# Performance work log

Hardware: AMD Instinct MI355X
Metric: run time of the kernel (lower is better)

## Reference

```python
import jax, jax.numpy as jnp
import numpy as np

B, S, D, F, E = 4, 2048, 1024, 4096, 8

def setup_inputs() -> dict:
    key = jax.random.key(0)
    ks = jax.random.split(key, 5)
    x = jax.random.normal(ks[0], (B, S, D), dtype=jnp.float32)
    router_w = jax.random.normal(ks[1], (D, E), dtype=jnp.float32) * (D ** -0.5)
    router_b = jnp.zeros((E,), dtype=jnp.float32)
    w1 = jax.random.normal(ks[2], (E, F, D), dtype=jnp.float32) * (D ** -0.5)
    b1 = jnp.zeros((E, F), dtype=jnp.float32)
    w2 = jax.random.normal(ks[3], (E, D, F), dtype=jnp.float32) * (F ** -0.5)
    b2 = jnp.zeros((E, D), dtype=jnp.float32)
    return {"x": x, "router_w": router_w, "router_b": router_b,
            "w1": w1, "b1": b1, "w2": w2, "b2": b2}

def reference(x, router_w, router_b, w1, b1, w2, b2):
    # Router: mean over sequence, linear, softmax -> [B, E]
    routing_probs = jax.nn.softmax(jnp.mean(x, axis=1) @ router_w + router_b, axis=-1)
    # SMEAR merge weights: mean over batch -> [E] (dropout is identity, p=0)
    ew = jnp.mean(routing_probs, axis=0)
    # Batched weighted sum of stacked expert parameters (fuses the python loop)
    mw1 = jnp.einsum('e,efd->fd', ew, w1)   # [F, D]
    mb1 = ew @ b1                            # [F]
    mw2 = jnp.einsum('e,edf->df', ew, w2)   # [D, F]
    mb2 = ew @ b2                            # [D]
    # functional_call on merged expert (MLP with GELU)
    h = jax.nn.gelu(jnp.einsum('bsd,fd->bsf', x, mw1) + mb1)
    out = jnp.einsum('bsf,df->bsd', h, mw2) + mb2
    return out
```

## Files before the change

kernel.cpp:

```cpp
#include <hip/hip_runtime.h>
#include <hip/hip_bf16.h>
#include <stdint.h>

#define B_ 4
#define S_ 2048
#define D_ 1024
#define F_ 4096
#define E_ 8

typedef __attribute__((ext_vector_type(4))) float f32x4;
typedef __attribute__((ext_vector_type(8))) short bf16x8;

__device__ __forceinline__ unsigned short f2bf(float f) {
    union { float f; unsigned int u; } v; v.f = f;
    unsigned int r = v.u + 0x7fffu + ((v.u >> 16) & 1u);
    return (unsigned short)(r >> 16);
}

__device__ __forceinline__ float gelu_tanh(float x) {
    const float c0 = 0.7978845608028654f;
    const float c1 = 0.044715f;
    float x3 = x * x * x;
    return 0.5f * x * (1.0f + tanhf(c0 * (x + c1 * x3)));
}

__global__ void prep_x_kernel(const float* __restrict__ x,
                              unsigned short* __restrict__ xb,
                              float* __restrict__ xsum) {
    const int b = blockIdx.y;
    const int t = threadIdx.x;
    const int d0 = t * 4;
    const float* xbase = x + (size_t)b * S_ * D_;
    unsigned short* obase = xb + (size_t)b * S_ * D_;
    float s0 = 0.f, s1 = 0.f, s2 = 0.f, s3 = 0.f;
    for (int s = blockIdx.x; s < S_; s += gridDim.x) {
        f32x4 v = *(const f32x4*)(xbase + (size_t)s * D_ + d0);
        ushort4 o;
        o.x = f2bf(v.x); o.y = f2bf(v.y); o.z = f2bf(v.z); o.w = f2bf(v.w);
        *(ushort4*)(obase + (size_t)s * D_ + d0) = o;
        s0 += v.x; s1 += v.y; s2 += v.z; s3 += v.w;
    }
    atomicAdd(&xsum[b * D_ + d0 + 0], s0);
    atomicAdd(&xsum[b * D_ + d0 + 1], s1);
    atomicAdd(&xsum[b * D_ + d0 + 2], s2);
    atomicAdd(&xsum[b * D_ + d0 + 3], s3);
}

__global__ void router_kernel(const float* __restrict__ xsum,
                              const float* __restrict__ rw,
                              const float* __restrict__ rb,
                              float* __restrict__ ew) {
    __shared__ float logits[B_][E_];
    __shared__ float probs[B_][E_];
    const int t = threadIdx.x;
    const int b = t >> 6;
    const int e = (t >> 3) & 7;
    const int part = t & 7;
    float s = 0.f;
    const int dbeg = part * (D_ / 8);
    for (int d = dbeg; d < dbeg + D_ / 8; ++d)
        s += xsum[b * D_ + d] * rw[d * E_ + e];
    s += __shfl_down(s, 4);
    s += __shfl_down(s, 2);
    s += __shfl_down(s, 1);
    if (part == 0) logits[b][e] = s * (1.0f / S_) + rb[e];
    __syncthreads();
    if (t < B_) {
        float mx = -1e30f;
        for (int j = 0; j < E_; ++j) mx = fmaxf(mx, logits[t][j]);
        float sum = 0.f;
        float ex[E_];
        for (int j = 0; j < E_; ++j) { ex[j] = expf(logits[t][j] - mx); sum += ex[j]; }
        for (int j = 0; j < E_; ++j) probs[t][j] = ex[j] / sum;
    }
    __syncthreads();
    if (t < E_) {
        float m = 0.f;
        for (int j = 0; j < B_; ++j) m += probs[j][t];
        ew[t] = m * (1.0f / B_);
    }
}

__global__ void merge_w_kernel(const float* __restrict__ w, const float* __restrict__ ew,
                               unsigned short* __restrict__ dst, int n) {
    float e[E_];
#pragma unroll
    for (int i = 0; i < E_; ++i) e[i] = ew[i];
    const size_t total = (size_t)n >> 2;
    for (size_t q = (size_t)blockIdx.x * blockDim.x + threadIdx.x; q < total;
         q += (size_t)gridDim.x * blockDim.x) {
        f32x4 acc = {0.f, 0.f, 0.f, 0.f};
#pragma unroll
        for (int i = 0; i < E_; ++i) {
            f32x4 v = *(const f32x4*)(w + (size_t)i * n + q * 4);
            acc += v * e[i];
        }
        ushort4 o;
        o.x = f2bf(acc.x); o.y = f2bf(acc.y); o.z = f2bf(acc.z); o.w = f2bf(acc.w);
        *(ushort4*)(dst + q * 4) = o;
    }
}

__global__ void merge_biases(const float* __restrict__ b1, const float* __restrict__ b2,
                             const float* __restrict__ ew,
                             float* __restrict__ mb1, float* __restrict__ mb2) {
    const int i = blockIdx.x * blockDim.x + threadIdx.x;
    float e[E_];
#pragma unroll
    for (int j = 0; j < E_; ++j) e[j] = ew[j];
    if (i < F_) {
        float a = 0.f;
#pragma unroll
        for (int j = 0; j < E_; ++j) a += e[j] * b1[(size_t)j * F_ + i];
        mb1[i] = a;
    } else if (i - F_ < D_) {
        const int i2 = i - F_;
        float a = 0.f;
#pragma unroll
        for (int j = 0; j < E_; ++j) a += e[j] * b2[(size_t)j * D_ + i2];
        mb2[i2] = a;
    }
}

__global__ void init_out_kernel(float* __restrict__ out, const float* __restrict__ mb2) {
    const size_t total_q = (size_t)B_ * S_ * D_ / 4;
    for (size_t q = (size_t)blockIdx.x * blockDim.x + threadIdx.x; q < total_q;
         q += (size_t)gridDim.x * blockDim.x) {
        ((f32x4*)out)[q] = ((const f32x4*)mb2)[q & (D_ / 4 - 1)];
    }
}

#define LGKM0() do { asm volatile("s_waitcnt lgkmcnt(0)" ::: "memory"); \
                     __builtin_amdgcn_sched_barrier(0); } while (0)
#define VMCNT(n) asm volatile("s_waitcnt vmcnt(" #n ")" ::: "memory")
#define BARRIER() __builtin_amdgcn_s_barrier()

template <int EPI>
__global__ __launch_bounds__(512, 2) void gemm256(const unsigned short* __restrict__ A,
                                                  const unsigned short* __restrict__ Bm,
                                                  const float* __restrict__ bias,
                                                  void* __restrict__ Cout0,
                                                  int M, int N, int K, int Klen) {
    __shared__ __align__(128) char lds[131072];
    const int tid = threadIdx.x;
    const int wave = tid >> 6, lane = tid & 63;
    const int wr = wave >> 2, wc = wave & 3;
    const int row0 = blockIdx.y * 256, col0 = blockIdx.x * 256;
    const int kt0 = blockIdx.z * Klen;
    const int NI = Klen / 128;

    const int c0 = tid, c1 = tid + 512;
    const int r0c = ((c0 >> 7) << 4) | ((c0 >> 2) & 15);
    const int k0c = (((c0 >> 6) & 1) << 5) | ((((c0 & 3) << 3) ^ (((c0 >> 5) & 1) << 4)));
    const int r1c = ((c1 >> 7) << 4) | ((c1 >> 2) & 15);
    const int k1c = (((c1 >> 6) & 1) << 5) | ((((c1 & 3) << 3) ^ (((c1 >> 5) & 1) << 4)));
    const size_t soff0 = (size_t)r0c * K + k0c;
    const size_t soff1 = (size_t)r1c * K + k1c;

    const unsigned short* pA0 = A + (size_t)row0 * K + kt0;
    const unsigned short* pA1 = pA0 + (size_t)128 * K;
    const unsigned short* pB0 = Bm + (size_t)col0 * K + kt0;
    const unsigned short* pB1 = pB0 + (size_t)128 * K;

    int lane_off = ((lane & 15) << 6) + ((lane >> 4) << 4);
    lane_off ^= (lane & 8) << 2;
    const int wrOff = wr * 16384;
    const int wcOff = 32768 + (wc >> 1) * 16384 + (wc & 1) * 8192;

    f32x4 acc[8][4];
#pragma unroll
    for (int m = 0; m < 8; ++m)
#pragma unroll
        for (int n = 0; n < 4; ++n) acc[m][n] = (f32x4){0.f, 0.f, 0.f, 0.f};
    bf16x8 aF[4][2], bF[4][2];

#define STAGE(ptr, ktb, ldsoff) do { \
    __builtin_amdgcn_global_load_lds((const __attribute__((address_space(1))) void*)((ptr) + (ktb) + soff0), \
        (__attribute__((address_space(3))) void*)(lds + (ldsoff) + wave * 1024), 16, 0, 0); \
    __builtin_amdgcn_global_load_lds((const __attribute__((address_space(1))) void*)((ptr) + (ktb) + soff1), \
        (__attribute__((address_space(3))) void*)(lds + (ldsoff) + wave * 1024 + 8192), 16, 0, 0); \
  } while (0)

#define RDA4(MB, BUFB) do { _Pragma("unroll") for (int m = 0; m < 4; ++m) { \
    aF[m][0] = *(const bf16x8*)(lds + (BUFB) + wrOff + ((MB) + m) * 2048 + lane_off); \
    aF[m][1] = *(const bf16x8*)(lds + (BUFB) + wrOff + ((MB) + m) * 2048 + 1024 + lane_off); } } while (0)

#define RDB2(NB, BUFB) do { _Pragma("unroll") for (int n = 0; n < 2; ++n) { \
    bF[(NB) + n][0] = *(const bf16x8*)(lds + (BUFB) + wcOff + ((NB) + n) * 2048 + lane_off); \
    bF[(NB) + n][1] = *(const bf16x8*)(lds + (BUFB) + wcOff + ((NB) + n) * 2048 + 1024 + lane_off); } } while (0)

#define MFMAQ(MB, NB) do { \
    __builtin_amdgcn_s_setprio(1); \
    _Pragma("unroll") for (int m = 0; m < 4; ++m) \
    _Pragma("unroll") for (int n = 0; n < 2; ++n) \
    _Pragma("unroll") for (int ks = 0; ks < 2; ++ks) \
      acc[(MB) + m][(NB) + n] = __builtin_amdgcn_mfma_f32_16x16x32_bf16( \
          aF[m][ks], bF[(NB) + n][ks], acc[(MB) + m][(NB) + n], 0, 0, 0); \
    __builtin_amdgcn_s_setprio(0); \
  } while (0)

    STAGE(pA0, 0, 0);
    STAGE(pA1, 0, 16384);
    STAGE(pB0, 0, 32768);
    STAGE(pB1, 0, 49152);
    STAGE(pB0, 64, 65536 + 32768);
    STAGE(pB1, 64, 65536 + 49152);

    for (int i = 0; i < NI; ++i) {
        const int t = 2 * i;
        const int ktN1 = (t + 1) * 64, ktN2 = (t + 2) * 64, ktN3 = (t + 3) * 64;
        const bool last = (i == NI - 1);

        VMCNT(4);
        BARRIER();
        RDA4(0, 0); RDB2(0, 0);
        STAGE(pA0, ktN1, 65536);
        LGKM0();
        MFMAQ(0, 0);
        RDB2(2, 0);
        STAGE(pA1, ktN1, 65536 + 16384);
        LGKM0();
        MFMAQ(0, 2);
        BARRIER();
        RDA4(4, 0);
        if (!last) STAGE(pB0, ktN2, 32768);
        LGKM0();
        MFMAQ(4, 2);
        if (!last) STAGE(pB1, ktN2, 49152);
        MFMAQ(4, 0);
        if (last) { VMCNT(0); } else { VMCNT(4); }
        BARRIER();
        RDA4(0, 65536); RDB2(0, 65536);
        if (!last) STAGE(pA0, ktN2, 0);
        LGKM0();
        MFMAQ(0, 0);
        RDB2(2, 65536);
        if (!last) STAGE(pA1, ktN2, 16384);
        LGKM0();
        MFMAQ(0, 2);
        BARRIER();
        RDA4(4, 65536);
        if (!last) STAGE(pB0, ktN3, 65536 + 32768);
        LGKM0();
        MFMAQ(4, 2);
        if (!last) STAGE(pB1, ktN3, 65536 + 49152);
        MFMAQ(4, 0);
    }

    const int fr = lane & 15, fq = lane >> 4;
    if (EPI == 0) {
        unsigned short* dst = (unsigned short*)Cout0;
#pragma unroll
        for (int n = 0; n < 4; ++n) {
            const int c = col0 + wc * 64 + n * 16 + fr;
            const float bv = bias[c];
#pragma unroll
            for (int m = 0; m < 8; ++m) {
                const int rb = row0 + wr * 128 + m * 16 + fq * 4;
#pragma unroll
                for (int v = 0; v < 4; ++v) {
                    float val = acc[m][n][v] + bv;
                    dst[(size_t)(rb + v) * N + c] = f2bf(gelu_tanh(val));
                }
            }
        }
    } else {
        float* dst = (float*)Cout0;
#pragma unroll
        for (int n = 0; n < 4; ++n) {
            const int c = col0 + wc * 64 + n * 16 + fr;
#pragma unroll
            for (int m = 0; m < 8; ++m) {
                const int rb = row0 + wr * 128 + m * 16 + fq * 4;
#pragma unroll
                for (int v = 0; v < 4; ++v)
                    atomicAdd(&dst[(size_t)(rb + v) * N + c], acc[m][n][v]);
            }
        }
    }
#undef STAGE
#undef RDA4
#undef RDB2
#undef MFMAQ
}

extern "C" void kernel_launch(void* const* d_in, const int* in_sizes, int n_in,
                              void* d_out, int out_size, void* d_ws, size_t ws_size,
                              hipStream_t stream) {
    const float* x  = (const float*)d_in[0];
    const float* rw = (const float*)d_in[1];
    const float* rb = (const float*)d_in[2];
    const float* w1 = (const float*)d_in[3];
    const float* b1 = (const float*)d_in[4];
    const float* w2 = (const float*)d_in[5];
    const float* b2 = (const float*)d_in[6];
    float* out = (float*)d_out;

    char* p = (char*)d_ws;
    auto take = [&](size_t bytes) { char* r = p; p += (bytes + 255) & ~(size_t)255; return r; };
    float* xsum          = (float*)take((size_t)B_ * D_ * sizeof(float));
    float* ew            = (float*)take(E_ * sizeof(float));
    float* mb1           = (float*)take(F_ * sizeof(float));
    float* mb2           = (float*)take(D_ * sizeof(float));
    unsigned short* xb   = (unsigned short*)take((size_t)B_ * S_ * D_ * 2);
    unsigned short* mw1b = (unsigned short*)take((size_t)F_ * D_ * 2);
    unsigned short* mw2b = (unsigned short*)take((size_t)D_ * F_ * 2);
    unsigned short* h    = (unsigned short*)take((size_t)B_ * S_ * F_ * 2);

    hipMemsetAsync(xsum, 0, (size_t)B_ * D_ * sizeof(float), stream);
    prep_x_kernel<<<dim3(128, B_), 256, 0, stream>>>(x, xb, xsum);
    router_kernel<<<1, 256, 0, stream>>>(xsum, rw, rb, ew);
    merge_w_kernel<<<2048, 256, 0, stream>>>(w1, ew, mw1b, F_ * D_);
    merge_w_kernel<<<2048, 256, 0, stream>>>(w2, ew, mw2b, D_ * F_);
    merge_biases<<<(F_ + D_) / 256, 256, 0, stream>>>(b1, b2, ew, mb1, mb2);
    init_out_kernel<<<2048, 256, 0, stream>>>(out, mb2);
    gemm256<0><<<dim3(F_ / 256, (B_ * S_) / 256, 1), 512, 0, stream>>>(
        xb, mw1b, mb1, h, B_ * S_, F_, D_, D_);
    gemm256<3><<<dim3(D_ / 256, (B_ * S_) / 256, 2), 512, 0, stream>>>(
        h, mw2b, nullptr, out, B_ * S_, D_, F_, F_ / 2);
}
```

Baseline: 564.2 us.

## Replace split-K atomic GEMM2 with 128-row tile GEMM, fuse merge kernels, swizzle blocks

Swaps the second GEMM's split-K atomicAdd scheme for a new 128x256 tile kernel that writes output plus bias directly, which removes the init_out pass and the atomic traffic. Both GEMMs gain an XCD-style workgroup swizzle aimed at better L2 reuse. The two weight merges and the bias merge are fused into one launch. GELU's tanhf is replaced by an exp-based formula. The smaller tile lowers per-block reuse, and the fast exp changes numerics slightly.

```diff
diff --git a/kernel.cpp b/kernel.cpp
--- a/kernel.cpp
+++ b/kernel.cpp
@@ -20,8 +20,9 @@
 __device__ __forceinline__ float gelu_tanh(float x) {
     const float c0 = 0.7978845608028654f;
     const float c1 = 0.044715f;
-    float x3 = x * x * x;
-    return 0.5f * x * (1.0f + tanhf(c0 * (x + c1 * x3)));
+    float u = c0 * (x + c1 * x * x * x);
+    float t = 1.0f - 2.0f / (__expf(2.0f * u) + 1.0f);
+    return 0.5f * x * (1.0f + t);
 }
 
 __global__ void prep_x_kernel(const float* __restrict__ x,
@@ -81,14 +82,23 @@
     }
 }
 
-__global__ void merge_w_kernel(const float* __restrict__ w, const float* __restrict__ ew,
-                               unsigned short* __restrict__ dst, int n) {
+__global__ void merge_all_kernel(const float* __restrict__ w1, const float* __restrict__ w2,
+                                 const float* __restrict__ b1, const float* __restrict__ b2,
+                                 const float* __restrict__ ew,
+                                 unsigned short* __restrict__ mw1b, unsigned short* __restrict__ mw2b,
+                                 float* __restrict__ mb1, float* __restrict__ mb2) {
     float e[E_];
 #pragma unroll
     for (int i = 0; i < E_; ++i) e[i] = ew[i];
-    const size_t total = (size_t)n >> 2;
-    for (size_t q = (size_t)blockIdx.x * blockDim.x + threadIdx.x; q < total;
-         q += (size_t)gridDim.x * blockDim.x) {
+    const size_t n = (size_t)F_ * D_;
+    const size_t nq = n >> 2;
+    const int half = gridDim.x >> 1;
+    const bool first = (int)blockIdx.x < half;
+    const float* w = first ? w1 : w2;
+    unsigned short* dst = first ? mw1b : mw2b;
+    const int bid = first ? blockIdx.x : blockIdx.x - half;
+    for (size_t q = (size_t)bid * blockDim.x + threadIdx.x; q < nq;
+         q += (size_t)half * blockDim.x) {
         f32x4 acc = {0.f, 0.f, 0.f, 0.f};
 #pragma unroll
         for (int i = 0; i < E_; ++i) {
@@ -99,34 +109,21 @@
         o.x = f2bf(acc.x); o.y = f2bf(acc.y); o.z = f2bf(acc.z); o.w = f2bf(acc.w);
         *(ushort4*)(dst + q * 4) = o;
     }
-}
-
-__global__ void merge_biases(const float* __restrict__ b1, const float* __restrict__ b2,
-                             const float* __restrict__ ew,
-                             float* __restrict__ mb1, float* __restrict__ mb2) {
-    const int i = blockIdx.x * blockDim.x + threadIdx.x;
-    float e[E_];
-#pragma unroll
-    for (int j = 0; j < E_; ++j) e[j] = ew[j];
-    if (i < F_) {
-        float a = 0.f;
-#pragma unroll
-        for (int j = 0; j < E_; ++j) a += e[j] * b1[(size_t)j * F_ + i];
-        mb1[i] = a;
-    } else if (i - F_ < D_) {
-        const int i2 = i - F_;
-        float a = 0.f;
-#pragma unroll
-        for (int j = 0; j < E_; ++j) a += e[j] * b2[(size_t)j * D_ + i2];
-        mb2[i2] = a;
-    }
-}
-
-__global__ void init_out_kernel(float* __restrict__ out, const float* __restrict__ mb2) {
-    const size_t total_q = (size_t)B_ * S_ * D_ / 4;
-    for (size_t q = (size_t)blockIdx.x * blockDim.x + threadIdx.x; q < total_q;
-         q += (size_t)gridDim.x * blockDim.x) {
-        ((f32x4*)out)[q] = ((const f32x4*)mb2)[q & (D_ / 4 - 1)];
+    if (blockIdx.x == gridDim.x - 1) {
+        for (int i = threadIdx.x; i < F_ + D_; i += blockDim.x) {
+            if (i < F_) {
+                float a = 0.f;
+#pragma unroll
+                for (int j = 0; j < E_; ++j) a += e[j] * b1[(size_t)j * F_ + i];
+                mb1[i] = a;
+            } else {
+                const int i2 = i - F_;
+                float a = 0.f;
+#pragma unroll
+                for (int j = 0; j < E_; ++j) a += e[j] * b2[(size_t)j * D_ + i2];
+                mb2[i2] = a;
+            }
+        }
     }
 }
 
@@ -135,19 +132,21 @@
 #define VMCNT(n) asm volatile("s_waitcnt vmcnt(" #n ")" ::: "memory")
 #define BARRIER() __builtin_amdgcn_s_barrier()
 
-template <int EPI>
 __global__ __launch_bounds__(512, 2) void gemm256(const unsigned short* __restrict__ A,
                                                   const unsigned short* __restrict__ Bm,
                                                   const float* __restrict__ bias,
-                                                  void* __restrict__ Cout0,
-                                                  int M, int N, int K, int Klen) {
+                                                  unsigned short* __restrict__ Cout,
+                                                  int M, int N, int K) {
     __shared__ __align__(128) char lds[131072];
     const int tid = threadIdx.x;
     const int wave = tid >> 6, lane = tid & 63;
     const int wr = wave >> 2, wc = wave & 3;
-    const int row0 = blockIdx.y * 256, col0 = blockIdx.x * 256;
-    const int kt0 = blockIdx.z * Klen;
-    const int NI = Klen / 128;
+    const int nbx = N / 256;
+    const int wg = blockIdx.y * nbx + blockIdx.x;
+    const int nwg = (M / 256) * nbx;
+    const int swz = (wg & 7) * (nwg >> 3) + (wg >> 3);
+    const int row0 = (swz / nbx) * 256, col0 = (swz % nbx) * 256;
+    const int NI = K / 128;
 
     const int c0 = tid, c1 = tid + 512;
     const int r0c = ((c0 >> 7) << 4) | ((c0 >> 2) & 15);
@@ -157,9 +156,9 @@
     const size_t soff0 = (size_t)r0c * K + k0c;
     const size_t soff1 = (size_t)r1c * K + k1c;
 
-    const unsigned short* pA0 = A + (size_t)row0 * K + kt0;
+    const unsigned short* pA0 = A + (size_t)row0 * K;
     const unsigned short* pA1 = pA0 + (size_t)128 * K;
-    const unsigned short* pB0 = Bm + (size_t)col0 * K + kt0;
+    const unsigned short* pB0 = Bm + (size_t)col0 * K;
     const unsigned short* pB1 = pB0 + (size_t)128 * K;
 
     int lane_off = ((lane & 15) << 6) + ((lane >> 4) << 4);
@@ -174,22 +173,22 @@
         for (int n = 0; n < 4; ++n) acc[m][n] = (f32x4){0.f, 0.f, 0.f, 0.f};
     bf16x8 aF[4][2], bF[4][2];
 
-#define STAGE(ptr, ktb, ldsoff) do { \
+#define STAGE6(ptr, ktb, ldsoff) do { \
     __builtin_amdgcn_global_load_lds((const __attribute__((address_space(1))) void*)((ptr) + (ktb) + soff0), \
         (__attribute__((address_space(3))) void*)(lds + (ldsoff) + wave * 1024), 16, 0, 0); \
     __builtin_amdgcn_global_load_lds((const __attribute__((address_space(1))) void*)((ptr) + (ktb) + soff1), \
         (__attribute__((address_space(3))) void*)(lds + (ldsoff) + wave * 1024 + 8192), 16, 0, 0); \
   } while (0)
 
-#define RDA4(MB, BUFB) do { _Pragma("unroll") for (int m = 0; m < 4; ++m) { \
+#define RDA46(MB, BUFB) do { _Pragma("unroll") for (int m = 0; m < 4; ++m) { \
     aF[m][0] = *(const bf16x8*)(lds + (BUFB) + wrOff + ((MB) + m) * 2048 + lane_off); \
     aF[m][1] = *(const bf16x8*)(lds + (BUFB) + wrOff + ((MB) + m) * 2048 + 1024 + lane_off); } } while (0)
 
-#define RDB2(NB, BUFB) do { _Pragma("unroll") for (int n = 0; n < 2; ++n) { \
+#define RDB26(NB, BUFB) do { _Pragma("unroll") for (int n = 0; n < 2; ++n) { \
     bF[(NB) + n][0] = *(const bf16x8*)(lds + (BUFB) + wcOff + ((NB) + n) * 2048 + lane_off); \
     bF[(NB) + n][1] = *(const bf16x8*)(lds + (BUFB) + wcOff + ((NB) + n) * 2048 + 1024 + lane_off); } } while (0)
 
-#define MFMAQ(MB, NB) do { \
+#define MFMAQ6(MB, NB) do { \
     __builtin_amdgcn_s_setprio(1); \
     _Pragma("unroll") for (int m = 0; m < 4; ++m) \
     _Pragma("unroll") for (int n = 0; n < 2; ++n) \
@@ -199,12 +198,12 @@
     __builtin_amdgcn_s_setprio(0); \
   } while (0)
 
-    STAGE(pA0, 0, 0);
-    STAGE(pA1, 0, 16384);
-    STAGE(pB0, 0, 32768);
-    STAGE(pB1, 0, 49152);
-    STAGE(pB0, 64, 65536 + 32768);
-    STAGE(pB1, 64, 65536 + 49152);
+    STAGE6(pA0, 0, 0);
+    STAGE6(pA1, 0, 16384);
+    STAGE6(pB0, 0, 32768);
+    STAGE6(pB1, 0, 49152);
+    STAGE6(pB0, 64, 65536 + 32768);
+    STAGE6(pB1, 64, 65536 + 49152);
 
     for (int i = 0; i < NI; ++i) {
         const int t = 2 * i;
@@ -213,75 +212,194 @@
 
         VMCNT(4);
         BARRIER();
-        RDA4(0, 0); RDB2(0, 0);
-        STAGE(pA0, ktN1, 65536);
-        LGKM0();
-        MFMAQ(0, 0);
-        RDB2(2, 0);
-        STAGE(pA1, ktN1, 65536 + 16384);
-        LGKM0();
-        MFMAQ(0, 2);
-        BARRIER();
-        RDA4(4, 0);
-        if (!last) STAGE(pB0, ktN2, 32768);
-        LGKM0();
-        MFMAQ(4, 2);
-        if (!last) STAGE(pB1, ktN2, 49152);
-        MFMAQ(4, 0);
+        RDA46(0, 0); RDB26(0, 0);
+        STAGE6(pA0, ktN1, 65536);
+        LGKM0();
+        MFMAQ6(0, 0);
+        RDB26(2, 0);
+        STAGE6(pA1, ktN1, 65536 + 16384);
+        LGKM0();
+        MFMAQ6(0, 2);
+        BARRIER();
+        RDA46(4, 0);
+        if (!last) STAGE6(pB0, ktN2, 32768);
+        LGKM0();
+        MFMAQ6(4, 2);
+        if (!last) STAGE6(pB1, ktN2, 49152);
+        MFMAQ6(4, 0);
         if (last) { VMCNT(0); } else { VMCNT(4); }
         BARRIER();
-        RDA4(0, 65536); RDB2(0, 65536);
-        if (!last) STAGE(pA0, ktN2, 0);
-        LGKM0();
-        MFMAQ(0, 0);
-        RDB2(2, 65536);
-        if (!last) STAGE(pA1, ktN2, 16384);
-        LGKM0();
-        MFMAQ(0, 2);
-        BARRIER();
-        RDA4(4, 65536);
-        if (!last) STAGE(pB0, ktN3, 65536 + 32768);
-        LGKM0();
-        MFMAQ(4, 2);
-        if (!last) STAGE(pB1, ktN3, 65536 + 49152);
-        MFMAQ(4, 0);
+        RDA46(0, 65536); RDB26(0, 65536);
+        if (!last) STAGE6(pA0, ktN2, 0);
+        LGKM0();
+        MFMAQ6(0, 0);
+        RDB26(2, 65536);
+        if (!last) STAGE6(pA1, ktN2, 16384);
+        LGKM0();
+        MFMAQ6(0, 2);
+        BARRIER();
+        RDA46(4, 65536);
+        if (!last) STAGE6(pB0, ktN3, 65536 + 32768);
+        LGKM0();
+        MFMAQ6(4, 2);
+        if (!last) STAGE6(pB1, ktN3, 65536 + 49152);
+        MFMAQ6(4, 0);
     }
 
     const int fr = lane & 15, fq = lane >> 4;
-    if (EPI == 0) {
-        unsigned short* dst = (unsigned short*)Cout0;
-#pragma unroll
-        for (int n = 0; n < 4; ++n) {
-            const int c = col0 + wc * 64 + n * 16 + fr;
-            const float bv = bias[c];
-#pragma unroll
-            for (int m = 0; m < 8; ++m) {
-                const int rb = row0 + wr * 128 + m * 16 + fq * 4;
-#pragma unroll
-                for (int v = 0; v < 4; ++v) {
-                    float val = acc[m][n][v] + bv;
-                    dst[(size_t)(rb + v) * N + c] = f2bf(gelu_tanh(val));
-                }
+#pragma unroll
+    for (int n = 0; n < 4; ++n) {
+        const int c = col0 + wc * 64 + n * 16 + fr;
+        const float bv = bias[c];
+#pragma unroll
+        for (int m = 0; m < 8; ++m) {
+            const int rb = row0 + wr * 128 + m * 16 + fq * 4;
+#pragma unroll
+            for (int v = 0; v < 4; ++v) {
+                float val = acc[m][n][v] + bv;
+                Cout[(size_t)(rb + v) * N + c] = f2bf(gelu_tanh(val));
             }
         }
-    } else {
-        float* dst = (float*)Cout0;
-#pragma unroll
-        for (int n = 0; n < 4; ++n) {
-            const int c = col0 + wc * 64 + n * 16 + fr;
-#pragma unroll
-            for (int m = 0; m < 8; ++m) {
-                const int rb = row0 + wr * 128 + m * 16 + fq * 4;
-#pragma unroll
-                for (int v = 0; v < 4; ++v)
-                    atomicAdd(&dst[(size_t)(rb + v) * N + c], acc[m][n][v]);
-            }
+    }
+#undef STAGE6
+#undef RDA46
+#undef RDB26
+#undef MFMAQ6
+}
+
+__global__ __launch_bounds__(512, 2) void gemm128(const unsigned short* __restrict__ A,
+                                                  const unsigned short* __restrict__ Bm,
+                                                  const float* __restrict__ bias,
+                                                  float* __restrict__ Cout,
+                                                  int M, int N, int K) {
+    __shared__ __align__(128) char lds[98304];
+    const int tid = threadIdx.x;
+    const int wave = tid >> 6, lane = tid & 63;
+    const int wr = wave >> 2, wc = wave & 3;
+    const int nbx = N / 256;
+    const int wg = blockIdx.y * nbx + blockIdx.x;
+    const int nwg = (M / 128) * nbx;
+    const int swz = (wg & 7) * (nwg >> 3) + (wg >> 3);
+    const int row0 = (swz / nbx) * 128, col0 = (swz % nbx) * 256;
+    const int NI = K / 128;
+
+    const int c0 = tid, c1 = tid + 512;
+    const int r0c = ((c0 >> 7) << 4) | ((c0 >> 2) & 15);
+    const int k0c = (((c0 >> 6) & 1) << 5) | ((((c0 & 3) << 3) ^ (((c0 >> 5) & 1) << 4)));
+    const int r1c = ((c1 >> 7) << 4) | ((c1 >> 2) & 15);
+    const int k1c = (((c1 >> 6) & 1) << 5) | ((((c1 & 3) << 3) ^ (((c1 >> 5) & 1) << 4)));
+    const size_t soff0 = (size_t)r0c * K + k0c;
+    const size_t soff1 = (size_t)r1c * K + k1c;
+
+    const unsigned short* pA  = A + (size_t)row0 * K;
+    const unsigned short* pB0 = Bm + (size_t)col0 * K;
+    const unsigned short* pB1 = pB0 + (size_t)128 * K;
+
+    int lane_off = ((lane & 15) << 6) + ((lane >> 4) << 4);
+    lane_off ^= (lane & 8) << 2;
+    const int wcOff = (wc >> 1) * 16384 + (wc & 1) * 8192;
+
+    f32x4 acc[4][4];
+#pragma unroll
+    for (int m = 0; m < 4; ++m)
+#pragma unroll
+        for (int n = 0; n < 4; ++n) acc[m][n] = (f32x4){0.f, 0.f, 0.f, 0.f};
+    bf16x8 aF[2][2], bF[4][2];
+
+#define A0OFF 0
+#define B0OFF 16384
+#define A1OFF 49152
+#define B1OFF 65536
+
+#define STAGE1(ptr, ktb, ldsoff) do { \
+    __builtin_amdgcn_global_load_lds((const __attribute__((address_space(1))) void*)((ptr) + (ktb) + soff0), \
+        (__attribute__((address_space(3))) void*)(lds + (ldsoff) + wave * 1024), 16, 0, 0); \
+    __builtin_amdgcn_global_load_lds((const __attribute__((address_space(1))) void*)((ptr) + (ktb) + soff1), \
+        (__attribute__((address_space(3))) void*)(lds + (ldsoff) + wave * 1024 + 8192), 16, 0, 0); \
+  } while (0)
+
+#define RDA2(MB, ABASE) do { _Pragma("unroll") for (int j = 0; j < 2; ++j) { \
+    aF[j][0] = *(const bf16x8*)(lds + (ABASE) + (wr * 4 + (MB) + j) * 2048 + lane_off); \
+    aF[j][1] = *(const bf16x8*)(lds + (ABASE) + (wr * 4 + (MB) + j) * 2048 + 1024 + lane_off); } } while (0)
+
+#define RDB2X(NB, BBASE) do { _Pragma("unroll") for (int n = 0; n < 2; ++n) { \
+    bF[(NB) + n][0] = *(const bf16x8*)(lds + (BBASE) + wcOff + ((NB) + n) * 2048 + lane_off); \
+    bF[(NB) + n][1] = *(const bf16x8*)(lds + (BBASE) + wcOff + ((NB) + n) * 2048 + 1024 + lane_off); } } while (0)
+
+#define MFMAQ2(MB, NB) do { \
+    __builtin_amdgcn_s_setprio(1); \
+    _Pragma("unroll") for (int j = 0; j < 2; ++j) \
+    _Pragma("unroll") for (int n = 0; n < 2; ++n) \
+    _Pragma("unroll") for (int ks = 0; ks < 2; ++ks) \
+      acc[(MB) + j][(NB) + n] = __builtin_amdgcn_mfma_f32_16x16x32_bf16( \
+          aF[j][ks], bF[(NB) + n][ks], acc[(MB) + j][(NB) + n], 0, 0, 0); \
+    __builtin_amdgcn_s_setprio(0); \
+  } while (0)
+
+    STAGE1(pA, 0, A0OFF);
+    STAGE1(pB0, 0, B0OFF);
+    STAGE1(pB1, 0, B0OFF + 16384);
+    STAGE1(pB0, 64, B1OFF);
+    STAGE1(pB1, 64, B1OFF + 16384);
+
+    for (int i = 0; i < NI; ++i) {
+        const int t = 2 * i;
+        const bool last = (i == NI - 1);
+        const int kA1 = (t + 1) * 64, kN2 = (t + 2) * 64, kN3 = (t + 3) * 64;
+
+        VMCNT(4);
+        BARRIER();
+        RDA2(0, A0OFF); RDB2X(0, B0OFF);
+        STAGE1(pA, kA1, A1OFF);
+        LGKM0();
+        MFMAQ2(0, 0);
+        RDB2X(2, B0OFF);
+        LGKM0();
+        MFMAQ2(0, 2);
+        BARRIER();
+        RDA2(2, A0OFF);
+        if (!last) { STAGE1(pB0, kN2, B0OFF); STAGE1(pB1, kN2, B0OFF + 16384); }
+        LGKM0();
+        MFMAQ2(2, 2);
+        MFMAQ2(2, 0);
+        if (last) { VMCNT(0); } else { VMCNT(4); }
+        BARRIER();
+        RDA2(0, A1OFF); RDB2X(0, B1OFF);
+        if (!last) STAGE1(pA, kN2, A0OFF);
+        LGKM0();
+        MFMAQ2(0, 0);
+        RDB2X(2, B1OFF);
+        LGKM0();
+        MFMAQ2(0, 2);
+        BARRIER();
+        RDA2(2, A1OFF);
+        if (!last) { STAGE1(pB0, kN3, B1OFF); STAGE1(pB1, kN3, B1OFF + 16384); }
+        LGKM0();
+        MFMAQ2(2, 2);
+        MFMAQ2(2, 0);
+    }
+
+    const int fr = lane & 15, fq = lane >> 4;
+#pragma unroll
+    for (int n = 0; n < 4; ++n) {
+        const int c = col0 + wc * 64 + n * 16 + fr;
+        const float bv = bias[c];
+#pragma unroll
+        for (int m = 0; m < 4; ++m) {
+            const int rb = row0 + wr * 64 + m * 16 + fq * 4;
+#pragma unroll
+            for (int v = 0; v < 4; ++v)
+                Cout[(size_t)(rb + v) * N + c] = acc[m][n][v] + bv;
         }
     }
-#undef STAGE
-#undef RDA4
-#undef RDB2
-#undef MFMAQ
+#undef STAGE1
+#undef RDA2
+#undef RDB2X
+#undef MFMAQ2
+#undef A0OFF
+#undef B0OFF
+#undef A1OFF
+#undef B1OFF
 }
 
 extern "C" void kernel_launch(void* const* d_in, const int* in_sizes, int n_in,
@@ -310,12 +428,9 @@
     hipMemsetAsync(xsum, 0, (size_t)B_ * D_ * sizeof(float), stream);
     prep_x_kernel<<<dim3(128, B_), 256, 0, stream>>>(x, xb, xsum);
     router_kernel<<<1, 256, 0, stream>>>(xsum, rw, rb, ew);
-    merge_w_kernel<<<2048, 256, 0, stream>>>(w1, ew, mw1b, F_ * D_);
-    merge_w_kernel<<<2048, 256, 0, stream>>>(w2, ew, mw2b, D_ * F_);
-    merge_biases<<<(F_ + D_) / 256, 256, 0, stream>>>(b1, b2, ew, mb1, mb2);
-    init_out_kernel<<<2048, 256, 0, stream>>>(out, mb2);
-    gemm256<0><<<dim3(F_ / 256, (B_ * S_) / 256, 1), 512, 0, stream>>>(
-        xb, mw1b, mb1, h, B_ * S_, F_, D_, D_);
-    gemm256<3><<<dim3(D_ / 256, (B_ * S_) / 256, 2), 512, 0, stream>>>(
-        h, mw2b, nullptr, out, B_ * S_, D_, F_, F_ / 2);
-}
+    merge_all_kernel<<<4096, 256, 0, stream>>>(w1, w2, b1, b2, ew, mw1b, mw2b, mb1, mb2);
+    gemm256<<<dim3(F_ / 256, (B_ * S_) / 256), 512, 0, stream>>>(
+        xb, mw1b, mb1, h, B_ * S_, F_, D_);
+    gemm128<<<dim3(D_ / 256, (B_ * S_) / 128), 512, 0, stream>>>(
+        h, mw2b, mb2, out, B_ * S_, D_, F_);
+}
```

Result: faster. 498.7 us (-11.6%).
